# Optimization experiments

Hardware: AMD Instinct MI355X
Metric: run time of the kernel (lower is better)

The kernel has to match this reference:

```python
import jax, jax.numpy as jnp
import numpy as np

DIM = 1536
DSTATE = 16


def setup_inputs() -> dict:
    key = jax.random.key(0)
    ks = jax.random.split(key, 8)
    batch, dim, seqlen, dstate = 4, DIM, 4096, DSTATE
    u = jax.random.normal(ks[0], (batch, dim, seqlen), dtype=jnp.float32)
    delta = jax.random.uniform(ks[1], (batch, dim, seqlen), dtype=jnp.float32)
    B = jax.random.normal(ks[2], (batch, dstate, seqlen), dtype=jnp.float32)
    C = jax.random.normal(ks[3], (batch, dstate, seqlen), dtype=jnp.float32)
    A = -jnp.exp(jax.random.normal(ks[4], (dim, dstate), dtype=jnp.float32))
    D = jax.random.normal(ks[5], (dim,), dtype=jnp.float32)
    delta_bias = jax.random.normal(ks[6], (dim,), dtype=jnp.float32)
    return {"u": u, "delta": delta, "B": B, "C": C, "A": A, "D": D, "delta_bias": delta_bias}


def _selective_scan(u, delta, B, C, A, D, delta_bias):
    # u, delta: [b, d, s]; B, C: [b, n, s]; A: [d, n]; D, delta_bias: [d]
    dt = jax.nn.softplus(delta + delta_bias[None, :, None])  # [b, d, s]
    # scan over time: carry x [b, d, n]
    dt_s = jnp.moveaxis(dt, 2, 0)   # [s, b, d]
    u_s = jnp.moveaxis(u, 2, 0)     # [s, b, d]
    B_s = jnp.moveaxis(B, 2, 0)     # [s, b, n]
    C_s = jnp.moveaxis(C, 2, 0)     # [s, b, n]

    def step(x, inp):
        dt_t, u_t, B_t, C_t = inp  # [b,d], [b,d], [b,n], [b,n]
        dA = jnp.exp(dt_t[..., None] * A[None])           # [b, d, n]
        dBu = (dt_t * u_t)[..., None] * B_t[:, None, :]   # [b, d, n]
        x = dA * x + dBu
        y = jnp.einsum('bdn,bn->bd', x, C_t) + D[None] * u_t
        return x, y

    b, d, s = u.shape
    n = A.shape[1]
    x0 = jnp.zeros((b, d, n), dtype=jnp.float32)
    _, ys = jax.lax.scan(step, x0, (dt_s, u_s, B_s, C_s))  # ys: [s, b, d]
    return jnp.moveaxis(ys, 0, 2)  # [b, d, s]


def reference(u, delta, B, C, A, D, delta_bias):
    return _selective_scan(u, delta, B, C, A, D, delta_bias)
```

## Files before the change

### kernel.cpp

```cpp
#include <hip/hip_runtime.h>

#define BATCH 4
#define DIM   1536
#define SEQ   4096
#define NST   16
#define NCH   32
#define CLEN  128
#define NCHAN (BATCH*DIM)
#define T     16
#define LSTR  17
#define WLDS  (64*LSTR)

#define LOG2E 1.4426950408889634f

__device__ __forceinline__ float softplus_f(float z) {
    return (z > 20.f) ? z : __logf(1.f + __expf(z));
}
__device__ __forceinline__ float exp2_hw(float z) {
    return __builtin_amdgcn_exp2f(z);
}

__global__ __launch_bounds__(256, 4) void ssm_phaseA(
    const float* __restrict__ u, const float* __restrict__ delta,
    const float* __restrict__ Bm, const float* __restrict__ A,
    const float* __restrict__ dbias,
    float* __restrict__ sumdt_out, float* __restrict__ S_out)
{
    __shared__ float lu[4 * WLDS];
    __shared__ float ld[4 * WLDS];
    __shared__ float lB[4 * T * NST];

    const int tid = threadIdx.x;
    const int w   = tid >> 6;
    const int l   = tid & 63;
    const int ch  = blockIdx.x * 256 + tid;
    const int d   = ch % DIM;
    const int bb  = (blockIdx.x * 256) / DIM;
    const int k   = blockIdx.y;
    const int s0  = k * CLEN;

    float* Lu = &lu[w * WLDS];
    float* Ld = &ld[w * WLDS];
    float* LB = &lB[w * T * NST];

    float A2[NST];
    const float* Ap = A + d * NST;
#pragma unroll
    for (int n = 0; n < NST; n++) A2[n] = Ap[n] * LOG2E;
    const float bias = dbias[d];

    const int coB = l >> 2;
    const int i4  = (l & 3) << 2;
    const size_t rowbase = (size_t)(blockIdx.x * 256 + w * 64) * SEQ + s0;
    const size_t bbase   = (size_t)(bb * NST + coB) * SEQ + s0;

    float4 ru[4], rd[4], rb;
#pragma unroll
    for (int q = 0; q < 4; q++) {
        const size_t g = rowbase + (size_t)(q * 16 + coB) * SEQ + i4;
        ru[q] = *(const float4*)(u + g);
        rd[q] = *(const float4*)(delta + g);
    }
    rb = *(const float4*)(Bm + bbase + i4);

    float S[NST];
#pragma unroll
    for (int n = 0; n < NST; n++) S[n] = 0.f;
    float sumdt = 0.f;

    for (int ss = 0; ss < CLEN; ss += T) {
#pragma unroll
        for (int q = 0; q < 4; q++) {
            float* pu = &Lu[(q * 16 + coB) * LSTR + i4];
            float* pd = &Ld[(q * 16 + coB) * LSTR + i4];
            pu[0] = ru[q].x; pu[1] = ru[q].y; pu[2] = ru[q].z; pu[3] = ru[q].w;
            pd[0] = rd[q].x; pd[1] = rd[q].y; pd[2] = rd[q].z; pd[3] = rd[q].w;
        }
        LB[(i4 + 0) * NST + coB] = rb.x;
        LB[(i4 + 1) * NST + coB] = rb.y;
        LB[(i4 + 2) * NST + coB] = rb.z;
        LB[(i4 + 3) * NST + coB] = rb.w;

        if (ss + T < CLEN) {
#pragma unroll
            for (int q = 0; q < 4; q++) {
                const size_t g = rowbase + (size_t)(q * 16 + coB) * SEQ + (ss + T) + i4;
                ru[q] = *(const float4*)(u + g);
                rd[q] = *(const float4*)(delta + g);
            }
            rb = *(const float4*)(Bm + bbase + (ss + T) + i4);
        }

        const float* lur = &Lu[l * LSTR];
        const float* ldr = &Ld[l * LSTR];
#pragma unroll
        for (int i = 0; i < T; i++) {
            const float uu  = lur[i];
            const float dt  = softplus_f(ldr[i] + bias);
            const float dtu = dt * uu;
            sumdt += dt;
            const float* bi = &LB[i * NST];
#pragma unroll
            for (int n = 0; n < NST; n++) {
                const float a = exp2_hw(dt * A2[n]);
                S[n] = fmaf(a, S[n], dtu * bi[n]);
            }
        }
    }

    const size_t base = ((size_t)k * NCHAN + ch) * NST;
#pragma unroll
    for (int n = 0; n < NST; n += 4)
        *(float4*)(S_out + base + n) = make_float4(S[n], S[n+1], S[n+2], S[n+3]);
    sumdt_out[(size_t)k * NCHAN + ch] = sumdt;
}

__global__ __launch_bounds__(256) void ssm_phaseB(
    const float* __restrict__ A, const float* __restrict__ sumdt,
    float* __restrict__ S)
{
    const int t  = blockIdx.x * 256 + threadIdx.x;
    const int n  = t & 15;
    const int ch = t >> 4;
    if (ch >= NCHAN) return;
    const int d = ch % DIM;
    const float An2 = A[d * NST + n] * LOG2E;
    float x = 0.f;
    for (int k = 0; k < NCH; k++) {
        const size_t idx = ((size_t)k * NCHAN + ch) * NST + n;
        const float s_old = S[idx];
        S[idx] = x;
        const float P = exp2_hw(An2 * sumdt[(size_t)k * NCHAN + ch]);
        x = fmaf(P, x, s_old);
    }
}

__global__ __launch_bounds__(256, 4) void ssm_phaseC(
    const float* __restrict__ u, const float* __restrict__ delta,
    const float* __restrict__ Bm, const float* __restrict__ Cm,
    const float* __restrict__ A, const float* __restrict__ Dv,
    const float* __restrict__ dbias, const float* __restrict__ x0,
    float* __restrict__ y)
{
    __shared__ float lu[4 * WLDS];
    __shared__ float ld[4 * WLDS];
    __shared__ float lB[4 * T * NST];
    __shared__ float lC[4 * T * NST];

    const int tid = threadIdx.x;
    const int w   = tid >> 6;
    const int l   = tid & 63;
    const int ch  = blockIdx.x * 256 + tid;
    const int d   = ch % DIM;
    const int bb  = (blockIdx.x * 256) / DIM;
    const int k   = blockIdx.y;
    const int s0  = k * CLEN;

    float* Lu = &lu[w * WLDS];
    float* Ld = &ld[w * WLDS];
    float* LB = &lB[w * T * NST];
    float* LC = &lC[w * T * NST];

    float A2[NST];
    const float* Ap = A + d * NST;
#pragma unroll
    for (int n = 0; n < NST; n++) A2[n] = Ap[n] * LOG2E;
    const float bias = dbias[d];
    const float Dval = Dv[d];

    float x[NST];
    const size_t xbase = ((size_t)k * NCHAN + ch) * NST;
#pragma unroll
    for (int n = 0; n < NST; n += 4) {
        const float4 xv = *(const float4*)(x0 + xbase + n);
        x[n] = xv.x; x[n+1] = xv.y; x[n+2] = xv.z; x[n+3] = xv.w;
    }

    const int coB = l >> 2;
    const int i4  = (l & 3) << 2;
    const size_t rowbase = (size_t)(blockIdx.x * 256 + w * 64) * SEQ + s0;
    const size_t bbase   = (size_t)(bb * NST + coB) * SEQ + s0;

    float4 ru[4], rd[4], rb, rc;
#pragma unroll
    for (int q = 0; q < 4; q++) {
        const size_t g = rowbase + (size_t)(q * 16 + coB) * SEQ + i4;
        ru[q] = *(const float4*)(u + g);
        rd[q] = *(const float4*)(delta + g);
    }
    rb = *(const float4*)(Bm + bbase + i4);
    rc = *(const float4*)(Cm + bbase + i4);

    for (int ss = 0; ss < CLEN; ss += T) {
#pragma unroll
        for (int q = 0; q < 4; q++) {
            float* pu = &Lu[(q * 16 + coB) * LSTR + i4];
            float* pd = &Ld[(q * 16 + coB) * LSTR + i4];
            pu[0] = ru[q].x; pu[1] = ru[q].y; pu[2] = ru[q].z; pu[3] = ru[q].w;
            pd[0] = rd[q].x; pd[1] = rd[q].y; pd[2] = rd[q].z; pd[3] = rd[q].w;
        }
        LB[(i4 + 0) * NST + coB] = rb.x;
        LB[(i4 + 1) * NST + coB] = rb.y;
        LB[(i4 + 2) * NST + coB] = rb.z;
        LB[(i4 + 3) * NST + coB] = rb.w;
        LC[(i4 + 0) * NST + coB] = rc.x;
        LC[(i4 + 1) * NST + coB] = rc.y;
        LC[(i4 + 2) * NST + coB] = rc.z;
        LC[(i4 + 3) * NST + coB] = rc.w;

        if (ss + T < CLEN) {
#pragma unroll
            for (int q = 0; q < 4; q++) {
                const size_t g = rowbase + (size_t)(q * 16 + coB) * SEQ + (ss + T) + i4;
                ru[q] = *(const float4*)(u + g);
                rd[q] = *(const float4*)(delta + g);
            }
            rb = *(const float4*)(Bm + bbase + (ss + T) + i4);
            rc = *(const float4*)(Cm + bbase + (ss + T) + i4);
        }

        float* lur = &Lu[l * LSTR];
        const float* ldr = &Ld[l * LSTR];
#pragma unroll
        for (int i = 0; i < T; i++) {
            const float uu  = lur[i];
            const float dt  = softplus_f(ldr[i] + bias);
            const float dtu = dt * uu;
            const float* bi = &LB[i * NST];
            const float* ci = &LC[i * NST];
            float acc = Dval * uu;
#pragma unroll
            for (int n = 0; n < NST; n++) {
                const float a = exp2_hw(dt * A2[n]);
                x[n] = fmaf(a, x[n], dtu * bi[n]);
                acc  = fmaf(x[n], ci[n], acc);
            }
            lur[i] = acc;
        }

#pragma unroll
        for (int q = 0; q < 4; q++) {
            const float* pr = &Lu[(q * 16 + coB) * LSTR + i4];
            *(float4*)(y + rowbase + (size_t)(q * 16 + coB) * SEQ + ss + i4) =
                make_float4(pr[0], pr[1], pr[2], pr[3]);
        }
    }
}

extern "C" void kernel_launch(void* const* d_in, const int* in_sizes, int n_in,
                              void* d_out, int out_size, void* d_ws, size_t ws_size,
                              hipStream_t stream)
{
    const float* u     = (const float*)d_in[0];
    const float* delta = (const float*)d_in[1];
    const float* Bm    = (const float*)d_in[2];
    const float* Cm    = (const float*)d_in[3];
    const float* A     = (const float*)d_in[4];
    const float* Dv    = (const float*)d_in[5];
    const float* dbias = (const float*)d_in[6];
    float* y = (float*)d_out;

    float* sumdt = (float*)d_ws;
    float* S     = sumdt + (size_t)NCHAN * NCH;

    const dim3 grid(NCHAN / 256, NCH);
    ssm_phaseA<<<grid, 256, 0, stream>>>(u, delta, Bm, A, dbias, sumdt, S);
    ssm_phaseB<<<(NCHAN * NST) / 256, 256, 0, stream>>>(A, sumdt, S);
    ssm_phaseC<<<grid, 256, 0, stream>>>(u, delta, Bm, Cm, A, Dv, dbias, S, y);
}
```

Baseline: 491.9 us.

## Shorten scan chunks, precompute softplus at LDS staging, raise occupancy

Switches to 64-step chunks when the workspace is large enough, which doubles the number of chunks and blocks for more parallelism. Raises the launch-bounds occupancy target to 6. Halves the LDS tile to 8 timesteps and computes softplus while staging delta into LDS, so each value is evaluated once with less redundancy in the inner loop. B and C loads are split across half-waves, and the phase-B carry loop prefetches its next values. In exchange, phase B gets a longer serial chain and the workspace holds more S traffic, and the tighter register budget may cause spills.

```diff
diff --git a/kernel.cpp b/kernel.cpp
--- a/kernel.cpp
+++ b/kernel.cpp
@@ -4,11 +4,10 @@
 #define DIM   1536
 #define SEQ   4096
 #define NST   16
-#define NCH   32
-#define CLEN  128
 #define NCHAN (BATCH*DIM)
-#define T     16
-#define LSTR  17
+
+#define T     8
+#define LSTR  9
 #define WLDS  (64*LSTR)
 
 #define LOG2E 1.4426950408889634f
@@ -20,7 +19,8 @@
     return __builtin_amdgcn_exp2f(z);
 }
 
-__global__ __launch_bounds__(256, 4) void ssm_phaseA(
+template<int CLEN>
+__global__ __launch_bounds__(256, 6) void ssm_phaseA(
     const float* __restrict__ u, const float* __restrict__ delta,
     const float* __restrict__ Bm, const float* __restrict__ A,
     const float* __restrict__ dbias,
@@ -47,21 +47,25 @@
     const float* Ap = A + d * NST;
 #pragma unroll
     for (int n = 0; n < NST; n++) A2[n] = Ap[n] * LOG2E;
-    const float bias = dbias[d];
-
-    const int coB = l >> 2;
-    const int i4  = (l & 3) << 2;
+
+    const int ro = l >> 1;
+    const int c4 = (l & 1) << 2;
+    const int dS = (blockIdx.x * 256 + w * 64) % DIM;
+    const float sb0 = dbias[dS + ro];
+    const float sb1 = dbias[dS + 32 + ro];
+
     const size_t rowbase = (size_t)(blockIdx.x * 256 + w * 64) * SEQ + s0;
-    const size_t bbase   = (size_t)(bb * NST + coB) * SEQ + s0;
-
-    float4 ru[4], rd[4], rb;
-#pragma unroll
-    for (int q = 0; q < 4; q++) {
-        const size_t g = rowbase + (size_t)(q * 16 + coB) * SEQ + i4;
+    const int nb = ro & 15;
+    const size_t bbase = (size_t)(bb * NST + nb) * SEQ + s0;
+
+    float4 ru[2], rd[2], rb;
+#pragma unroll
+    for (int q = 0; q < 2; q++) {
+        const size_t g = rowbase + (size_t)(q * 32 + ro) * SEQ + c4;
         ru[q] = *(const float4*)(u + g);
         rd[q] = *(const float4*)(delta + g);
     }
-    rb = *(const float4*)(Bm + bbase + i4);
+    if (l < 32) rb = *(const float4*)(Bm + bbase + c4);
 
     float S[NST];
 #pragma unroll
@@ -70,25 +74,31 @@
 
     for (int ss = 0; ss < CLEN; ss += T) {
 #pragma unroll
-        for (int q = 0; q < 4; q++) {
-            float* pu = &Lu[(q * 16 + coB) * LSTR + i4];
-            float* pd = &Ld[(q * 16 + coB) * LSTR + i4];
+        for (int q = 0; q < 2; q++) {
+            const float sb = q ? sb1 : sb0;
+            float* pu = &Lu[(q * 32 + ro) * LSTR + c4];
+            float* pd = &Ld[(q * 32 + ro) * LSTR + c4];
             pu[0] = ru[q].x; pu[1] = ru[q].y; pu[2] = ru[q].z; pu[3] = ru[q].w;
-            pd[0] = rd[q].x; pd[1] = rd[q].y; pd[2] = rd[q].z; pd[3] = rd[q].w;
-        }
-        LB[(i4 + 0) * NST + coB] = rb.x;
-        LB[(i4 + 1) * NST + coB] = rb.y;
-        LB[(i4 + 2) * NST + coB] = rb.z;
-        LB[(i4 + 3) * NST + coB] = rb.w;
+            pd[0] = softplus_f(rd[q].x + sb);
+            pd[1] = softplus_f(rd[q].y + sb);
+            pd[2] = softplus_f(rd[q].z + sb);
+            pd[3] = softplus_f(rd[q].w + sb);
+        }
+        if (l < 32) {
+            LB[(c4 + 0) * NST + nb] = rb.x;
+            LB[(c4 + 1) * NST + nb] = rb.y;
+            LB[(c4 + 2) * NST + nb] = rb.z;
+            LB[(c4 + 3) * NST + nb] = rb.w;
+        }
 
         if (ss + T < CLEN) {
 #pragma unroll
-            for (int q = 0; q < 4; q++) {
-                const size_t g = rowbase + (size_t)(q * 16 + coB) * SEQ + (ss + T) + i4;
+            for (int q = 0; q < 2; q++) {
+                const size_t g = rowbase + (size_t)(q * 32 + ro) * SEQ + (ss + T) + c4;
                 ru[q] = *(const float4*)(u + g);
                 rd[q] = *(const float4*)(delta + g);
             }
-            rb = *(const float4*)(Bm + bbase + (ss + T) + i4);
+            if (l < 32) rb = *(const float4*)(Bm + bbase + (ss + T) + c4);
         }
 
         const float* lur = &Lu[l * LSTR];
@@ -96,7 +106,7 @@
 #pragma unroll
         for (int i = 0; i < T; i++) {
             const float uu  = lur[i];
-            const float dt  = softplus_f(ldr[i] + bias);
+            const float dt  = ldr[i];
             const float dtu = dt * uu;
             sumdt += dt;
             const float* bi = &LB[i * NST];
@@ -115,6 +125,7 @@
     sumdt_out[(size_t)k * NCHAN + ch] = sumdt;
 }
 
+template<int NCH>
 __global__ __launch_bounds__(256) void ssm_phaseB(
     const float* __restrict__ A, const float* __restrict__ sumdt,
     float* __restrict__ S)
@@ -125,17 +136,29 @@
     if (ch >= NCHAN) return;
     const int d = ch % DIM;
     const float An2 = A[d * NST + n] * LOG2E;
+
+    const size_t kstride = (size_t)NCHAN * NST;
+    size_t idx = (size_t)ch * NST + n;
+
     float x = 0.f;
+    float s_nxt = S[idx];
+    float p_nxt = sumdt[ch];
+#pragma unroll 4
     for (int k = 0; k < NCH; k++) {
-        const size_t idx = ((size_t)k * NCHAN + ch) * NST + n;
-        const float s_old = S[idx];
+        const float s_old = s_nxt;
+        const float pdt   = p_nxt;
+        if (k + 1 < NCH) {
+            s_nxt = S[idx + kstride];
+            p_nxt = sumdt[(size_t)(k + 1) * NCHAN + ch];
+        }
         S[idx] = x;
-        const float P = exp2_hw(An2 * sumdt[(size_t)k * NCHAN + ch]);
-        x = fmaf(P, x, s_old);
-    }
-}
-
-__global__ __launch_bounds__(256, 4) void ssm_phaseC(
+        x = fmaf(exp2_hw(An2 * pdt), x, s_old);
+        idx += kstride;
+    }
+}
+
+template<int CLEN>
+__global__ __launch_bounds__(256, 6) void ssm_phaseC(
     const float* __restrict__ u, const float* __restrict__ delta,
     const float* __restrict__ Bm, const float* __restrict__ Cm,
     const float* __restrict__ A, const float* __restrict__ Dv,
@@ -165,7 +188,6 @@
     const float* Ap = A + d * NST;
 #pragma unroll
     for (int n = 0; n < NST; n++) A2[n] = Ap[n] * LOG2E;
-    const float bias = dbias[d];
     const float Dval = Dv[d];
 
     float x[NST];
@@ -176,47 +198,54 @@
         x[n] = xv.x; x[n+1] = xv.y; x[n+2] = xv.z; x[n+3] = xv.w;
     }
 
-    const int coB = l >> 2;
-    const int i4  = (l & 3) << 2;
+    const int ro = l >> 1;
+    const int c4 = (l & 1) << 2;
+    const int dS = (blockIdx.x * 256 + w * 64) % DIM;
+    const float sb0 = dbias[dS + ro];
+    const float sb1 = dbias[dS + 32 + ro];
+
     const size_t rowbase = (size_t)(blockIdx.x * 256 + w * 64) * SEQ + s0;
-    const size_t bbase   = (size_t)(bb * NST + coB) * SEQ + s0;
-
-    float4 ru[4], rd[4], rb, rc;
-#pragma unroll
-    for (int q = 0; q < 4; q++) {
-        const size_t g = rowbase + (size_t)(q * 16 + coB) * SEQ + i4;
+    const int nb = ro & 15;
+    const float* BC = (l < 32) ? Bm : Cm;
+    const size_t bbase = (size_t)(bb * NST + nb) * SEQ + s0;
+
+    float4 ru[2], rd[2], rbc;
+#pragma unroll
+    for (int q = 0; q < 2; q++) {
+        const size_t g = rowbase + (size_t)(q * 32 + ro) * SEQ + c4;
         ru[q] = *(const float4*)(u + g);
         rd[q] = *(const float4*)(delta + g);
     }
-    rb = *(const float4*)(Bm + bbase + i4);
-    rc = *(const float4*)(Cm + bbase + i4);
+    rbc = *(const float4*)(BC + bbase + c4);
 
     for (int ss = 0; ss < CLEN; ss += T) {
 #pragma unroll
-        for (int q = 0; q < 4; q++) {
-            float* pu = &Lu[(q * 16 + coB) * LSTR + i4];
-            float* pd = &Ld[(q * 16 + coB) * LSTR + i4];
+        for (int q = 0; q < 2; q++) {
+            const float sb = q ? sb1 : sb0;
+            float* pu = &Lu[(q * 32 + ro) * LSTR + c4];
+            float* pd = &Ld[(q * 32 + ro) * LSTR + c4];
             pu[0] = ru[q].x; pu[1] = ru[q].y; pu[2] = ru[q].z; pu[3] = ru[q].w;
-            pd[0] = rd[q].x; pd[1] = rd[q].y; pd[2] = rd[q].z; pd[3] = rd[q].w;
-        }
-        LB[(i4 + 0) * NST + coB] = rb.x;
-        LB[(i4 + 1) * NST + coB] = rb.y;
-        LB[(i4 + 2) * NST + coB] = rb.z;
-        LB[(i4 + 3) * NST + coB] = rb.w;
-        LC[(i4 + 0) * NST + coB] = rc.x;
-        LC[(i4 + 1) * NST + coB] = rc.y;
-        LC[(i4 + 2) * NST + coB] = rc.z;
-        LC[(i4 + 3) * NST + coB] = rc.w;
+            pd[0] = softplus_f(rd[q].x + sb);
+            pd[1] = softplus_f(rd[q].y + sb);
+            pd[2] = softplus_f(rd[q].z + sb);
+            pd[3] = softplus_f(rd[q].w + sb);
+        }
+        {
+            float* dst = (l < 32) ? LB : LC;
+            dst[(c4 + 0) * NST + nb] = rbc.x;
+            dst[(c4 + 1) * NST + nb] = rbc.y;
+            dst[(c4 + 2) * NST + nb] = rbc.z;
+            dst[(c4 + 3) * NST + nb] = rbc.w;
+        }
 
         if (ss + T < CLEN) {
 #pragma unroll
-            for (int q = 0; q < 4; q++) {
-                const size_t g = rowbase + (size_t)(q * 16 + coB) * SEQ + (ss + T) + i4;
+            for (int q = 0; q < 2; q++) {
+                const size_t g = rowbase + (size_t)(q * 32 + ro) * SEQ + (ss + T) + c4;
                 ru[q] = *(const float4*)(u + g);
                 rd[q] = *(const float4*)(delta + g);
             }
-            rb = *(const float4*)(Bm + bbase + (ss + T) + i4);
-            rc = *(const float4*)(Cm + bbase + (ss + T) + i4);
+            rbc = *(const float4*)(BC + bbase + (ss + T) + c4);
         }
 
         float* lur = &Lu[l * LSTR];
@@ -224,7 +253,7 @@
 #pragma unroll
         for (int i = 0; i < T; i++) {
             const float uu  = lur[i];
-            const float dt  = softplus_f(ldr[i] + bias);
+            const float dt  = ldr[i];
             const float dtu = dt * uu;
             const float* bi = &LB[i * NST];
             const float* ci = &LC[i * NST];
@@ -239,12 +268,28 @@
         }
 
 #pragma unroll
-        for (int q = 0; q < 4; q++) {
-            const float* pr = &Lu[(q * 16 + coB) * LSTR + i4];
-            *(float4*)(y + rowbase + (size_t)(q * 16 + coB) * SEQ + ss + i4) =
+        for (int q = 0; q < 2; q++) {
+            const float* pr = &Lu[(q * 32 + ro) * LSTR + c4];
+            *(float4*)(y + rowbase + (size_t)(q * 32 + ro) * SEQ + ss + c4) =
                 make_float4(pr[0], pr[1], pr[2], pr[3]);
         }
     }
+}
+
+template<int CLEN>
+static void run_pipeline(const float* u, const float* delta, const float* Bm,
+                         const float* Cm, const float* A, const float* Dv,
+                         const float* dbias, float* y, float* ws,
+                         hipStream_t stream)
+{
+    constexpr int NCH = SEQ / CLEN;
+    float* sumdt = ws;
+    float* S     = ws + (size_t)NCH * NCHAN;
+
+    const dim3 grid(NCHAN / 256, NCH);
+    ssm_phaseA<CLEN><<<grid, 256, 0, stream>>>(u, delta, Bm, A, dbias, sumdt, S);
+    ssm_phaseB<NCH><<<(NCHAN * NST) / 256, 256, 0, stream>>>(A, sumdt, S);
+    ssm_phaseC<CLEN><<<grid, 256, 0, stream>>>(u, delta, Bm, Cm, A, Dv, dbias, S, y);
 }
 
 extern "C" void kernel_launch(void* const* d_in, const int* in_sizes, int n_in,
@@ -258,13 +303,13 @@
     const float* A     = (const float*)d_in[4];
     const float* Dv    = (const float*)d_in[5];
     const float* dbias = (const float*)d_in[6];
-    float* y = (float*)d_out;
-
-    float* sumdt = (float*)d_ws;
-    float* S     = sumdt + (size_t)NCHAN * NCH;
-
-    const dim3 grid(NCHAN / 256, NCH);
-    ssm_phaseA<<<grid, 256, 0, stream>>>(u, delta, Bm, A, dbias, sumdt, S);
-    ssm_phaseB<<<(NCHAN * NST) / 256, 256, 0, stream>>>(A, sumdt, S);
-    ssm_phaseC<<<grid, 256, 0, stream>>>(u, delta, Bm, Cm, A, Dv, dbias, S, y);
-}
+    float* y  = (float*)d_out;
+    float* ws = (float*)d_ws;
+
+    const size_t need64 = ((size_t)64 * NCHAN + (size_t)64 * NCHAN * NST) * sizeof(float);
+    if (ws_size >= need64) {
+        run_pipeline<64>(u, delta, Bm, Cm, A, Dv, dbias, y, ws, stream);
+    } else {
+        run_pipeline<128>(u, delta, Bm, Cm, A, Dv, dbias, y, ws, stream);
+    }
+}
```

Measured after the change: 1.023 ms. 2.08x slower.

## Split each channel's 16 states across a 4-lane quad with DPP broadcasts

Applied to the files above, without the earlier changes.

Phases A and C now assign four lanes per channel, each holding four of the sixteen state elements. Per-timestep dt and u values are broadcast within the quad using DPP moves, and the C·x dot product is reduced with a quad DPP sum. This removes the per-thread 16-wide state arrays and the LDS staging of u and delta, which cuts register pressure (launch bounds raised to 6) and quadruples the block count. In exchange, softplus is computed once per element by its owning lane, but the exp2 work is unchanged and cross-lane shuffles are added. Phase B also gets software prefetching of S and sumdt.

```diff
diff --git a/kernel.cpp b/kernel.cpp
--- a/kernel.cpp
+++ b/kernel.cpp
@@ -4,12 +4,11 @@
 #define DIM   1536
 #define SEQ   4096
 #define NST   16
+#define NCHAN (BATCH*DIM)
 #define NCH   32
 #define CLEN  128
-#define NCHAN (BATCH*DIM)
 #define T     16
-#define LSTR  17
-#define WLDS  (64*LSTR)
+#define LBSTR 20
 
 #define LOG2E 1.4426950408889634f
 
@@ -20,99 +19,99 @@
     return __builtin_amdgcn_exp2f(z);
 }
 
-__global__ __launch_bounds__(256, 4) void ssm_phaseA(
+template<int CTRL>
+__device__ __forceinline__ float dpp_qp(float v) {
+    return __int_as_float(
+        __builtin_amdgcn_mov_dpp(__float_as_int(v), CTRL, 0xf, 0xf, true));
+}
+__device__ __forceinline__ float quad_sum(float v) {
+    v += dpp_qp<0xB1>(v);
+    v += dpp_qp<0x4E>(v);
+    return v;
+}
+
+
+__global__ __launch_bounds__(256, 6) void ssm_phaseA(
     const float* __restrict__ u, const float* __restrict__ delta,
     const float* __restrict__ Bm, const float* __restrict__ A,
     const float* __restrict__ dbias,
     float* __restrict__ sumdt_out, float* __restrict__ S_out)
 {
-    __shared__ float lu[4 * WLDS];
-    __shared__ float ld[4 * WLDS];
-    __shared__ float lB[4 * T * NST];
+    __shared__ float lB[4 * T * LBSTR];
 
     const int tid = threadIdx.x;
     const int w   = tid >> 6;
     const int l   = tid & 63;
-    const int ch  = blockIdx.x * 256 + tid;
+    const int q   = l >> 2;
+    const int sub = l & 3;
+    const int cj  = sub << 2;
+
+    const int ch0 = blockIdx.x * 64;
+    const int ch  = ch0 + w * 16 + q;
     const int d   = ch % DIM;
-    const int bb  = (blockIdx.x * 256) / DIM;
+    const int bb  = ch0 / DIM;
     const int k   = blockIdx.y;
     const int s0  = k * CLEN;
 
-    float* Lu = &lu[w * WLDS];
-    float* Ld = &ld[w * WLDS];
-    float* LB = &lB[w * T * NST];
-
-    float A2[NST];
-    const float* Ap = A + d * NST;
-#pragma unroll
-    for (int n = 0; n < NST; n++) A2[n] = Ap[n] * LOG2E;
-    const float bias = dbias[d];
-
-    const int coB = l >> 2;
-    const int i4  = (l & 3) << 2;
-    const size_t rowbase = (size_t)(blockIdx.x * 256 + w * 64) * SEQ + s0;
-    const size_t bbase   = (size_t)(bb * NST + coB) * SEQ + s0;
-
-    float4 ru[4], rd[4], rb;
-#pragma unroll
-    for (int q = 0; q < 4; q++) {
-        const size_t g = rowbase + (size_t)(q * 16 + coB) * SEQ + i4;
-        ru[q] = *(const float4*)(u + g);
-        rd[q] = *(const float4*)(delta + g);
-    }
-    rb = *(const float4*)(Bm + bbase + i4);
-
-    float S[NST];
-#pragma unroll
-    for (int n = 0; n < NST; n++) S[n] = 0.f;
+    float* LB = &lB[w * T * LBSTR];
+
+    float A2[4];
+    {
+        const float4 av = *(const float4*)(A + (size_t)d * NST + sub * 4);
+        A2[0] = av.x * LOG2E; A2[1] = av.y * LOG2E;
+        A2[2] = av.z * LOG2E; A2[3] = av.w * LOG2E;
+    }
+    const float sbias = dbias[d];
+
+    const size_t ubase = (size_t)ch * SEQ + s0;
+    const size_t bbase = ((size_t)bb * NST + q) * SEQ + s0;
+
+    float4 run = *(const float4*)(u + ubase + cj);
+    float4 rdn = *(const float4*)(delta + ubase + cj);
+    float4 rbn = *(const float4*)(Bm + bbase + cj);
+
+    float S[4] = {0.f, 0.f, 0.f, 0.f};
     float sumdt = 0.f;
 
     for (int ss = 0; ss < CLEN; ss += T) {
-#pragma unroll
-        for (int q = 0; q < 4; q++) {
-            float* pu = &Lu[(q * 16 + coB) * LSTR + i4];
-            float* pd = &Ld[(q * 16 + coB) * LSTR + i4];
-            pu[0] = ru[q].x; pu[1] = ru[q].y; pu[2] = ru[q].z; pu[3] = ru[q].w;
-            pd[0] = rd[q].x; pd[1] = rd[q].y; pd[2] = rd[q].z; pd[3] = rd[q].w;
+        const float uc[4] = {run.x, run.y, run.z, run.w};
+        const float dc[4] = {softplus_f(rdn.x + sbias), softplus_f(rdn.y + sbias),
+                             softplus_f(rdn.z + sbias), softplus_f(rdn.w + sbias)};
+        sumdt += (dc[0] + dc[1]) + (dc[2] + dc[3]);
+
+        LB[(cj + 0) * LBSTR + q] = rbn.x;
+        LB[(cj + 1) * LBSTR + q] = rbn.y;
+        LB[(cj + 2) * LBSTR + q] = rbn.z;
+        LB[(cj + 3) * LBSTR + q] = rbn.w;
+
+        if (ss + T < CLEN) {
+            run = *(const float4*)(u + ubase + (ss + T) + cj);
+            rdn = *(const float4*)(delta + ubase + (ss + T) + cj);
+            rbn = *(const float4*)(Bm + bbase + (ss + T) + cj);
         }
-        LB[(i4 + 0) * NST + coB] = rb.x;
-        LB[(i4 + 1) * NST + coB] = rb.y;
-        LB[(i4 + 2) * NST + coB] = rb.z;
-        LB[(i4 + 3) * NST + coB] = rb.w;
-
-        if (ss + T < CLEN) {
-#pragma unroll
-            for (int q = 0; q < 4; q++) {
-                const size_t g = rowbase + (size_t)(q * 16 + coB) * SEQ + (ss + T) + i4;
-                ru[q] = *(const float4*)(u + g);
-                rd[q] = *(const float4*)(delta + g);
-            }
-            rb = *(const float4*)(Bm + bbase + (ss + T) + i4);
-        }
-
-        const float* lur = &Lu[l * LSTR];
-        const float* ldr = &Ld[l * LSTR];
-#pragma unroll
-        for (int i = 0; i < T; i++) {
-            const float uu  = lur[i];
-            const float dt  = softplus_f(ldr[i] + bias);
-            const float dtu = dt * uu;
-            sumdt += dt;
-            const float* bi = &LB[i * NST];
-#pragma unroll
-            for (int n = 0; n < NST; n++) {
-                const float a = exp2_hw(dt * A2[n]);
-                S[n] = fmaf(a, S[n], dtu * bi[n]);
-            }
-        }
-    }
-
-    const size_t base = ((size_t)k * NCHAN + ch) * NST;
-#pragma unroll
-    for (int n = 0; n < NST; n += 4)
-        *(float4*)(S_out + base + n) = make_float4(S[n], S[n+1], S[n+2], S[n+3]);
-    sumdt_out[(size_t)k * NCHAN + ch] = sumdt;
+
+#define ASTEP(ii) { \
+        const float dt  = dpp_qp<(((ii) >> 2) * 0x55)>(dc[(ii) & 3]); \
+        const float uu  = dpp_qp<(((ii) >> 2) * 0x55)>(uc[(ii) & 3]); \
+        const float dtu = dt * uu; \
+        const float4 bv = *(const float4*)(&LB[(ii) * LBSTR + cj]); \
+        S[0] = fmaf(exp2_hw(dt * A2[0]), S[0], dtu * bv.x); \
+        S[1] = fmaf(exp2_hw(dt * A2[1]), S[1], dtu * bv.y); \
+        S[2] = fmaf(exp2_hw(dt * A2[2]), S[2], dtu * bv.z); \
+        S[3] = fmaf(exp2_hw(dt * A2[3]), S[3], dtu * bv.w); \
+    }
+        ASTEP(0)  ASTEP(1)  ASTEP(2)  ASTEP(3)
+        ASTEP(4)  ASTEP(5)  ASTEP(6)  ASTEP(7)
+        ASTEP(8)  ASTEP(9)  ASTEP(10) ASTEP(11)
+        ASTEP(12) ASTEP(13) ASTEP(14) ASTEP(15)
+#undef ASTEP
+    }
+
+    *(float4*)(S_out + ((size_t)k * NCHAN + ch) * NST + sub * 4) =
+        make_float4(S[0], S[1], S[2], S[3]);
+
+    const float sfull = quad_sum(sumdt);
+    if (sub == 0) sumdt_out[(size_t)k * NCHAN + ch] = sfull;
 }
 
 __global__ __launch_bounds__(256) void ssm_phaseB(
@@ -124,126 +123,127 @@
     const int ch = t >> 4;
     if (ch >= NCHAN) return;
     const int d = ch % DIM;
-    const float An2 = A[d * NST + n] * LOG2E;
+    const float An2 = A[(size_t)d * NST + n] * LOG2E;
+
+    const size_t kstride = (size_t)NCHAN * NST;
+    size_t idx = (size_t)ch * NST + n;
+
     float x = 0.f;
+    float s_nxt = S[idx];
+    float p_nxt = sumdt[ch];
+#pragma unroll 4
     for (int k = 0; k < NCH; k++) {
-        const size_t idx = ((size_t)k * NCHAN + ch) * NST + n;
-        const float s_old = S[idx];
+        const float s_old = s_nxt;
+        const float pdt   = p_nxt;
+        if (k + 1 < NCH) {
+            s_nxt = S[idx + kstride];
+            p_nxt = sumdt[(size_t)(k + 1) * NCHAN + ch];
+        }
         S[idx] = x;
-        const float P = exp2_hw(An2 * sumdt[(size_t)k * NCHAN + ch]);
-        x = fmaf(P, x, s_old);
-    }
-}
-
-__global__ __launch_bounds__(256, 4) void ssm_phaseC(
+        x = fmaf(exp2_hw(An2 * pdt), x, s_old);
+        idx += kstride;
+    }
+}
+
+__global__ __launch_bounds__(256, 6) void ssm_phaseC(
     const float* __restrict__ u, const float* __restrict__ delta,
     const float* __restrict__ Bm, const float* __restrict__ Cm,
     const float* __restrict__ A, const float* __restrict__ Dv,
     const float* __restrict__ dbias, const float* __restrict__ x0,
     float* __restrict__ y)
 {
-    __shared__ float lu[4 * WLDS];
-    __shared__ float ld[4 * WLDS];
-    __shared__ float lB[4 * T * NST];
-    __shared__ float lC[4 * T * NST];
+    __shared__ float lB[4 * T * LBSTR];
+    __shared__ float lC[4 * T * LBSTR];
 
     const int tid = threadIdx.x;
     const int w   = tid >> 6;
     const int l   = tid & 63;
-    const int ch  = blockIdx.x * 256 + tid;
+    const int q   = l >> 2;
+    const int sub = l & 3;
+    const int cj  = sub << 2;
+
+    const int ch0 = blockIdx.x * 64;
+    const int ch  = ch0 + w * 16 + q;
     const int d   = ch % DIM;
-    const int bb  = (blockIdx.x * 256) / DIM;
+    const int bb  = ch0 / DIM;
     const int k   = blockIdx.y;
     const int s0  = k * CLEN;
 
-    float* Lu = &lu[w * WLDS];
-    float* Ld = &ld[w * WLDS];
-    float* LB = &lB[w * T * NST];
-    float* LC = &lC[w * T * NST];
-
-    float A2[NST];
-    const float* Ap = A + d * NST;
-#pragma unroll
-    for (int n = 0; n < NST; n++) A2[n] = Ap[n] * LOG2E;
-    const float bias = dbias[d];
-    const float Dval = Dv[d];
-
-    float x[NST];
-    const size_t xbase = ((size_t)k * NCHAN + ch) * NST;
-#pragma unroll
-    for (int n = 0; n < NST; n += 4) {
-        const float4 xv = *(const float4*)(x0 + xbase + n);
-        x[n] = xv.x; x[n+1] = xv.y; x[n+2] = xv.z; x[n+3] = xv.w;
-    }
-
-    const int coB = l >> 2;
-    const int i4  = (l & 3) << 2;
-    const size_t rowbase = (size_t)(blockIdx.x * 256 + w * 64) * SEQ + s0;
-    const size_t bbase   = (size_t)(bb * NST + coB) * SEQ + s0;
-
-    float4 ru[4], rd[4], rb, rc;
-#pragma unroll
-    for (int q = 0; q < 4; q++) {
-        const size_t g = rowbase + (size_t)(q * 16 + coB) * SEQ + i4;
-        ru[q] = *(const float4*)(u + g);
-        rd[q] = *(const float4*)(delta + g);
-    }
-    rb = *(const float4*)(Bm + bbase + i4);
-    rc = *(const float4*)(Cm + bbase + i4);
+    float* LB = &lB[w * T * LBSTR];
+    float* LC = &lC[w * T * LBSTR];
+
+    float A2[4];
+    {
+        const float4 av = *(const float4*)(A + (size_t)d * NST + sub * 4);
+        A2[0] = av.x * LOG2E; A2[1] = av.y * LOG2E;
+        A2[2] = av.z * LOG2E; A2[3] = av.w * LOG2E;
+    }
+    const float sbias = dbias[d];
+    const float Dval  = Dv[d];
+
+    float x[4];
+    {
+        const float4 xv = *(const float4*)(x0 + ((size_t)k * NCHAN + ch) * NST + sub * 4);
+        x[0] = xv.x; x[1] = xv.y; x[2] = xv.z; x[3] = xv.w;
+    }
+
+    const size_t ubase = (size_t)ch * SEQ + s0;
+    const size_t bbase = ((size_t)bb * NST + q) * SEQ + s0;
+
+    float4 run = *(const float4*)(u + ubase + cj);
+    float4 rdn = *(const float4*)(delta + ubase + cj);
+    float4 rbn = *(const float4*)(Bm + bbase + cj);
+    float4 rcn = *(const float4*)(Cm + bbase + cj);
 
     for (int ss = 0; ss < CLEN; ss += T) {
-#pragma unroll
-        for (int q = 0; q < 4; q++) {
-            float* pu = &Lu[(q * 16 + coB) * LSTR + i4];
-            float* pd = &Ld[(q * 16 + coB) * LSTR + i4];
-            pu[0] = ru[q].x; pu[1] = ru[q].y; pu[2] = ru[q].z; pu[3] = ru[q].w;
-            pd[0] = rd[q].x; pd[1] = rd[q].y; pd[2] = rd[q].z; pd[3] = rd[q].w;
+        const float uc[4] = {run.x, run.y, run.z, run.w};
+        const float dc[4] = {softplus_f(rdn.x + sbias), softplus_f(rdn.y + sbias),
+                             softplus_f(rdn.z + sbias), softplus_f(rdn.w + sbias)};
+
+        LB[(cj + 0) * LBSTR + q] = rbn.x;
+        LB[(cj + 1) * LBSTR + q] = rbn.y;
+        LB[(cj + 2) * LBSTR + q] = rbn.z;
+        LB[(cj + 3) * LBSTR + q] = rbn.w;
+        LC[(cj + 0) * LBSTR + q] = rcn.x;
+        LC[(cj + 1) * LBSTR + q] = rcn.y;
+        LC[(cj + 2) * LBSTR + q] = rcn.z;
+        LC[(cj + 3) * LBSTR + q] = rcn.w;
+
+        if (ss + T < CLEN) {
+            run = *(const float4*)(u + ubase + (ss + T) + cj);
+            rdn = *(const float4*)(delta + ubase + (ss + T) + cj);
+            rbn = *(const float4*)(Bm + bbase + (ss + T) + cj);
+            rcn = *(const float4*)(Cm + bbase + (ss + T) + cj);
         }
-        LB[(i4 + 0) * NST + coB] = rb.x;
-        LB[(i4 + 1) * NST + coB] = rb.y;
-        LB[(i4 + 2) * NST + coB] = rb.z;
-        LB[(i4 + 3) * NST + coB] = rb.w;
-        LC[(i4 + 0) * NST + coB] = rc.x;
-        LC[(i4 + 1) * NST + coB] = rc.y;
-        LC[(i4 + 2) * NST + coB] = rc.z;
-        LC[(i4 + 3) * NST + coB] = rc.w;
-
-        if (ss + T < CLEN) {
-#pragma unroll
-            for (int q = 0; q < 4; q++) {
-                const size_t g = rowbase + (size_t)(q * 16 + coB) * SEQ + (ss + T) + i4;
-                ru[q] = *(const float4*)(u + g);
-                rd[q] = *(const float4*)(delta + g);
-            }
-            rb = *(const float4*)(Bm + bbase + (ss + T) + i4);
-            rc = *(const float4*)(Cm + bbase + (ss + T) + i4);
-        }
-
-        float* lur = &Lu[l * LSTR];
-        const float* ldr = &Ld[l * LSTR];
-#pragma unroll
-        for (int i = 0; i < T; i++) {
-            const float uu  = lur[i];
-            const float dt  = softplus_f(ldr[i] + bias);
-            const float dtu = dt * uu;
-            const float* bi = &LB[i * NST];
-            const float* ci = &LC[i * NST];
-            float acc = Dval * uu;
-#pragma unroll
-            for (int n = 0; n < NST; n++) {
-                const float a = exp2_hw(dt * A2[n]);
-                x[n] = fmaf(a, x[n], dtu * bi[n]);
-                acc  = fmaf(x[n], ci[n], acc);
-            }
-            lur[i] = acc;
-        }
-
-#pragma unroll
-        for (int q = 0; q < 4; q++) {
-            const float* pr = &Lu[(q * 16 + coB) * LSTR + i4];
-            *(float4*)(y + rowbase + (size_t)(q * 16 + coB) * SEQ + ss + i4) =
-                make_float4(pr[0], pr[1], pr[2], pr[3]);
-        }
+
+        float yreg[4];
+
+#define CSTEP(ii) { \
+        const float dt  = dpp_qp<(((ii) >> 2) * 0x55)>(dc[(ii) & 3]); \
+        const float uu  = dpp_qp<(((ii) >> 2) * 0x55)>(uc[(ii) & 3]); \
+        const float dtu = dt * uu; \
+        const float4 bv = *(const float4*)(&LB[(ii) * LBSTR + cj]); \
+        const float4 cv = *(const float4*)(&LC[(ii) * LBSTR + cj]); \
+        x[0] = fmaf(exp2_hw(dt * A2[0]), x[0], dtu * bv.x); \
+        x[1] = fmaf(exp2_hw(dt * A2[1]), x[1], dtu * bv.y); \
+        x[2] = fmaf(exp2_hw(dt * A2[2]), x[2], dtu * bv.z); \
+        x[3] = fmaf(exp2_hw(dt * A2[3]), x[3], dtu * bv.w); \
+        float acc = x[0] * cv.x; \
+        acc = fmaf(x[1], cv.y, acc); \
+        acc = fmaf(x[2], cv.z, acc); \
+        acc = fmaf(x[3], cv.w, acc); \
+        acc = quad_sum(acc); \
+        const float yv = fmaf(Dval, uu, acc); \
+        if (sub == ((ii) >> 2)) yreg[(ii) & 3] = yv; \
+    }
+        CSTEP(0)  CSTEP(1)  CSTEP(2)  CSTEP(3)
+        CSTEP(4)  CSTEP(5)  CSTEP(6)  CSTEP(7)
+        CSTEP(8)  CSTEP(9)  CSTEP(10) CSTEP(11)
+        CSTEP(12) CSTEP(13) CSTEP(14) CSTEP(15)
+#undef CSTEP
+
+        *(float4*)(y + ubase + ss + sub * 4) =
+            make_float4(yreg[0], yreg[1], yreg[2], yreg[3]);
     }
 }
 
@@ -263,7 +263,7 @@
     float* sumdt = (float*)d_ws;
     float* S     = sumdt + (size_t)NCHAN * NCH;
 
-    const dim3 grid(NCHAN / 256, NCH);
+    const dim3 grid(NCHAN / 64, NCH);
     ssm_phaseA<<<grid, 256, 0, stream>>>(u, delta, Bm, A, dbias, sumdt, S);
     ssm_phaseB<<<(NCHAN * NST) / 256, 256, 0, stream>>>(A, sumdt, S);
     ssm_phaseC<<<grid, 256, 0, stream>>>(u, delta, Bm, Cm, A, Dv, dbias, S, y);
```

Result: slower. 537.6 us (+9.3%).
